# Kernel tuning notes

Measured on AMD Instinct MI355X. Metric: run time of the kernel, lower is better.

## Reference

```python
import jax, jax.numpy as jnp
import numpy as np

K = 7            # involution kernel size
GC = 16          # group_channels (hardcoded in module)
EPS = 1e-5       # BatchNorm eps


def setup_inputs() -> dict:
    key = jax.random.key(0)
    ks = jax.random.split(key, 5)
    C, R = 256, 4
    mid = C // R                      # 64
    groups = C // GC                  # 16
    B, H, W = 4, 56, 56
    x = jax.random.normal(ks[0], (B, C, H, W), dtype=jnp.float32)
    w1 = jax.random.normal(ks[1], (mid, C), dtype=jnp.float32) * (1.0 / np.sqrt(C))
    b1 = jax.random.normal(ks[2], (mid,), dtype=jnp.float32) * 0.01
    gamma = jnp.ones((mid,), dtype=jnp.float32)
    beta = jnp.zeros((mid,), dtype=jnp.float32)
    w2 = jax.random.normal(ks[3], (K * K * groups, mid), dtype=jnp.float32) * (1.0 / np.sqrt(mid))
    b2 = jax.random.normal(ks[4], (K * K * groups,), dtype=jnp.float32) * 0.01
    return {"x": x, "w1": w1, "b1": b1, "gamma": gamma, "beta": beta, "w2": w2, "b2": b2}


def reference(x, w1, b1, gamma, beta, w2, b2):
    B, C, H, W = x.shape
    groups = C // GC
    k2 = K * K
    pad = (K - 1) // 2

    # weight branch: 1x1 conv -> BN (batch stats, training-mode math) -> ReLU -> 1x1 conv
    t = jnp.einsum('oc,bchw->bohw', w1, x) + b1[None, :, None, None]
    mu = t.mean(axis=(0, 2, 3), keepdims=True)
    var = ((t - mu) ** 2).mean(axis=(0, 2, 3), keepdims=True)
    t = (t - mu) * jax.lax.rsqrt(var + EPS)
    t = t * gamma[None, :, None, None] + beta[None, :, None, None]
    t = jax.nn.relu(t)
    wgt = jnp.einsum('ot,bthw->bohw', w2, t) + b2[None, :, None, None]
    wgt = wgt.reshape(B, groups, k2, H, W)              # per-pixel kernels

    # unfold: kernel positions row-major (i over kh, j over kw), channel-major layout
    xp = jnp.pad(x, ((0, 0), (0, 0), (pad, pad), (pad, pad)))
    patches = jnp.stack(
        [xp[:, :, i:i + H, j:j + W] for i in range(K) for j in range(K)], axis=2
    )                                                   # [B, C, k2, H, W]
    patches = patches.reshape(B, groups, GC, k2, H, W)

    out = jnp.einsum('bgkhw,bgckhw->bgchw', wgt, patches)  # weighted sum over k2
    return out.reshape(B, C, H, W)
```

## Files before the change

kernel.cpp:

```cpp
#include <hip/hip_runtime.h>

#define KSZ   7
#define KK    49
#define GCH   16
#define CIN   256
#define MID   64
#define NGRP  16
#define WID   56
#define HWSZ  3136
#define NB    4
#define NPIX  (NB * HWSZ)
#define EPSV  1e-5f


__global__ __launch_bounds__(256) void k1_conv1(const float* __restrict__ x,
                                                const float* __restrict__ w1,
                                                const float* __restrict__ b1,
                                                float* __restrict__ ws) {
    const int tid = threadIdx.x;
    const int pix = blockIdx.x * 256 + tid;
    const int ob  = blockIdx.y * 4;
    const int b   = pix / HWSZ;
    const int hw  = pix - b * HWSZ;

    float acc[4];
#pragma unroll
    for (int i = 0; i < 4; ++i) acc[i] = b1[ob + i];

    const float* xp = x + (size_t)b * CIN * HWSZ + hw;
#pragma unroll 16
    for (int c = 0; c < CIN; ++c) {
        const float xv = xp[(size_t)c * HWSZ];
#pragma unroll
        for (int i = 0; i < 4; ++i)
            acc[i] = fmaf(w1[(ob + i) * CIN + c], xv, acc[i]);
    }

    float* tp = ws + 256 + (size_t)ob * NPIX + pix;
#pragma unroll
    for (int i = 0; i < 4; ++i) tp[(size_t)i * NPIX] = acc[i];

    __shared__ float bs[4];
    __shared__ float bq[4];
    if (tid < 4) { bs[tid] = 0.f; bq[tid] = 0.f; }
    __syncthreads();

#pragma unroll
    for (int i = 0; i < 4; ++i) {
        float s = acc[i];
        float q = acc[i] * acc[i];
#pragma unroll
        for (int m = 1; m < 64; m <<= 1) {
            s += __shfl_xor(s, m, 64);
            q += __shfl_xor(q, m, 64);
        }
        if ((tid & 63) == 0) {
            atomicAdd(&bs[i], s);
            atomicAdd(&bq[i], q);
        }
    }
    __syncthreads();
    if (tid < 4) {
        atomicAdd(&ws[ob + tid],      bs[tid]);
        atomicAdd(&ws[64 + ob + tid], bq[tid]);
    }
}

__global__ void k2_stats(float* __restrict__ ws,
                         const float* __restrict__ gamma,
                         const float* __restrict__ beta) {
    const int o = threadIdx.x;
    const float n   = (float)NPIX;
    const float mu  = ws[o] / n;
    const float var = ws[64 + o] / n - mu * mu;
    const float a   = gamma[o] * rsqrtf(var + EPSV);
    ws[128 + o] = a;
    ws[192 + o] = beta[o] - mu * a;
}

__global__ __launch_bounds__(256) void k3_fused(const float* __restrict__ x,
                                                const float* __restrict__ w2,
                                                const float* __restrict__ b2,
                                                const float* __restrict__ ws,
                                                float* __restrict__ out) {
    __shared__ float tl[MID][128];
    const int tid  = threadIdx.x;
    const int p    = tid & 127;
    const int half = __builtin_amdgcn_readfirstlane(tid >> 7);
    const int pix  = blockIdx.x * 128 + p;
    const int g    = blockIdx.y * 2 + half;
    const int b    = pix / HWSZ;
    const int hw   = pix - b * HWSZ;
    const int h    = hw / WID;
    const int w    = hw - h * WID;

    {
        const float* tcol = ws + 256 + blockIdx.x * 128 + p;
#pragma unroll 8
        for (int i = 0; i < 32; ++i) {
            const int o = half * 32 + i;
            const float v = tcol[(size_t)o * NPIX];
            tl[o][p] = fmaxf(0.f, fmaf(ws[128 + o], v, ws[192 + o]));
        }
    }
    __syncthreads();

    float acc[GCH];
#pragma unroll
    for (int cc = 0; cc < GCH; ++cc) acc[cc] = 0.f;

    const float* w2g = w2 + (size_t)g * KK * MID;
    const float* b2g = b2 + (size_t)g * KK;
    const int   xbase = (b * CIN + g * GCH) * HWSZ;

    for (int kc = 0; kc < 7; ++kc) {
        float aw[7];
#pragma unroll
        for (int j = 0; j < 7; ++j) aw[j] = b2g[kc * 7 + j];

#pragma unroll 8
        for (int o = 0; o < MID; ++o) {
            const float tv = tl[o][p];
#pragma unroll
            for (int j = 0; j < 7; ++j)
                aw[j] = fmaf(w2g[(kc * 7 + j) * MID + o], tv, aw[j]);
        }

        const int  hh    = h + kc - 3;
        const bool rowok = (unsigned)hh < 56u;
#pragma unroll
        for (int j = 0; j < 7; ++j) {
            const int  ww = w + j - 3;
            const bool ok = rowok && ((unsigned)ww < 56u);
            const float wm = ok ? aw[j] : 0.f;
            const int  off = ok ? (hh * WID + ww) : 0;
            const float* xb = x + xbase + off;
#pragma unroll
            for (int cc = 0; cc < GCH; ++cc)
                acc[cc] = fmaf(wm, xb[(size_t)cc * HWSZ], acc[cc]);
        }
    }

    float* ob = out + (size_t)xbase + hw;
#pragma unroll
    for (int cc = 0; cc < GCH; ++cc) ob[(size_t)cc * HWSZ] = acc[cc];
}

extern "C" void kernel_launch(void* const* d_in, const int* in_sizes, int n_in,
                              void* d_out, int out_size, void* d_ws, size_t ws_size,
                              hipStream_t stream) {
    const float* x     = (const float*)d_in[0];
    const float* w1    = (const float*)d_in[1];
    const float* b1    = (const float*)d_in[2];
    const float* gamma = (const float*)d_in[3];
    const float* beta  = (const float*)d_in[4];
    const float* w2    = (const float*)d_in[5];
    const float* b2    = (const float*)d_in[6];
    float* out = (float*)d_out;
    float* ws  = (float*)d_ws;

    hipMemsetAsync(ws, 0, 128 * sizeof(float), stream);

    k1_conv1<<<dim3(49, 16), 256, 0, stream>>>(x, w1, b1, ws);
    k2_stats<<<1, 64, 0, stream>>>(ws, gamma, beta);
    k3_fused<<<dim3(98, 8), 256, 0, stream>>>(x, w2, b2, ws, out);
}
```

Before: 104.0 us.

## Split involution kernel generation and aggregation across four waves via shared memory

Each block now handles one group with 512 threads. The four 128-thread quarters first compute disjoint slices of the 49 per-pixel kernel weights into shared memory. After a barrier, each quarter aggregates 4 of the group's 16 channels using those shared weights. This spreads the per-thread work of the second 1x1 conv and raises parallelism, at the cost of more shared memory (about 57KB per block), an extra barrier, and reloading the relu'd t tile per group.

```diff
diff --git a/kernel.cpp b/kernel.cpp
--- a/kernel.cpp
+++ b/kernel.cpp
@@ -78,72 +78,88 @@
     ws[192 + o] = beta[o] - mu * a;
 }
 
-__global__ __launch_bounds__(256) void k3_fused(const float* __restrict__ x,
+template <int T0, int NT>
+__device__ inline void phaseA(const float* __restrict__ w2g,
+                              const float* __restrict__ b2g,
+                              const float (*__restrict__ tl)[128],
+                              float (*__restrict__ wgt)[128], int p) {
+    float aw[NT];
+#pragma unroll
+    for (int t = 0; t < NT; ++t) aw[t] = b2g[T0 + t];
+#pragma unroll
+    for (int oc = 0; oc < MID; oc += 8) {
+        float tv[8];
+#pragma unroll
+        for (int i = 0; i < 8; ++i) tv[i] = tl[oc + i][p];
+#pragma unroll
+        for (int t = 0; t < NT; ++t)
+#pragma unroll
+            for (int i = 0; i < 8; ++i)
+                aw[t] = fmaf(w2g[(T0 + t) * MID + oc + i], tv[i], aw[t]);
+    }
+#pragma unroll
+    for (int t = 0; t < NT; ++t) wgt[T0 + t][p] = aw[t];
+}
+
+__global__ __launch_bounds__(512) void k3_fused(const float* __restrict__ x,
                                                 const float* __restrict__ w2,
                                                 const float* __restrict__ b2,
                                                 const float* __restrict__ ws,
                                                 float* __restrict__ out) {
     __shared__ float tl[MID][128];
-    const int tid  = threadIdx.x;
-    const int p    = tid & 127;
-    const int half = __builtin_amdgcn_readfirstlane(tid >> 7);
-    const int pix  = blockIdx.x * 128 + p;
-    const int g    = blockIdx.y * 2 + half;
-    const int b    = pix / HWSZ;
-    const int hw   = pix - b * HWSZ;
-    const int h    = hw / WID;
-    const int w    = hw - h * WID;
+    __shared__ float wgt[KK][128];
+    const int tid = threadIdx.x;
+    const int p   = tid & 127;
+    const int q   = __builtin_amdgcn_readfirstlane(tid >> 7);
+    const int pix = blockIdx.x * 128 + p;
+    const int g   = blockIdx.y;
+    const int b   = pix / HWSZ;
+    const int hw  = pix - b * HWSZ;
+    const int h   = hw / WID;
+    const int w   = hw - h * WID;
 
     {
         const float* tcol = ws + 256 + blockIdx.x * 128 + p;
-#pragma unroll 8
-        for (int i = 0; i < 32; ++i) {
-            const int o = half * 32 + i;
+#pragma unroll
+        for (int i = 0; i < 16; ++i) {
+            const int o = q * 16 + i;
             const float v = tcol[(size_t)o * NPIX];
             tl[o][p] = fmaxf(0.f, fmaf(ws[128 + o], v, ws[192 + o]));
         }
     }
     __syncthreads();
 
-    float acc[GCH];
-#pragma unroll
-    for (int cc = 0; cc < GCH; ++cc) acc[cc] = 0.f;
-
     const float* w2g = w2 + (size_t)g * KK * MID;
     const float* b2g = b2 + (size_t)g * KK;
-    const int   xbase = (b * CIN + g * GCH) * HWSZ;
 
-    for (int kc = 0; kc < 7; ++kc) {
-        float aw[7];
+    if      (q == 0) phaseA< 0, 12>(w2g, b2g, tl, wgt, p);
+    else if (q == 1) phaseA<12, 12>(w2g, b2g, tl, wgt, p);
+    else if (q == 2) phaseA<24, 12>(w2g, b2g, tl, wgt, p);
+    else             phaseA<36, 13>(w2g, b2g, tl, wgt, p);
+    __syncthreads();
+
+    float acc[4] = {0.f, 0.f, 0.f, 0.f};
+    const int xbase = (b * CIN + g * GCH + q * 4) * HWSZ;
+
 #pragma unroll
-        for (int j = 0; j < 7; ++j) aw[j] = b2g[kc * 7 + j];
-
-#pragma unroll 8
-        for (int o = 0; o < MID; ++o) {
-            const float tv = tl[o][p];
+    for (int t = 0; t < KK; ++t) {
+        const int di = t / 7 - 3;
+        const int dj = t % 7 - 3;
+        const int hh = h + di;
+        const int ww = w + dj;
+        const bool ok = ((unsigned)hh < 56u) && ((unsigned)ww < 56u);
+        const float wv = wgt[t][p];
+        const float wm = ok ? wv : 0.f;
+        const int  off = ok ? (hh * WID + ww) : 0;
+        const float* xb = x + xbase + off;
 #pragma unroll
-            for (int j = 0; j < 7; ++j)
-                aw[j] = fmaf(w2g[(kc * 7 + j) * MID + o], tv, aw[j]);
-        }
-
-        const int  hh    = h + kc - 3;
-        const bool rowok = (unsigned)hh < 56u;
-#pragma unroll
-        for (int j = 0; j < 7; ++j) {
-            const int  ww = w + j - 3;
-            const bool ok = rowok && ((unsigned)ww < 56u);
-            const float wm = ok ? aw[j] : 0.f;
-            const int  off = ok ? (hh * WID + ww) : 0;
-            const float* xb = x + xbase + off;
-#pragma unroll
-            for (int cc = 0; cc < GCH; ++cc)
-                acc[cc] = fmaf(wm, xb[(size_t)cc * HWSZ], acc[cc]);
-        }
+        for (int cc = 0; cc < 4; ++cc)
+            acc[cc] = fmaf(wm, xb[(size_t)cc * HWSZ], acc[cc]);
     }
 
     float* ob = out + (size_t)xbase + hw;
 #pragma unroll
-    for (int cc = 0; cc < GCH; ++cc) ob[(size_t)cc * HWSZ] = acc[cc];
+    for (int cc = 0; cc < 4; ++cc) ob[(size_t)cc * HWSZ] = acc[cc];
 }
 
 extern "C" void kernel_launch(void* const* d_in, const int* in_sizes, int n_in,
@@ -163,5 +179,5 @@
 
     k1_conv1<<<dim3(49, 16), 256, 0, stream>>>(x, w1, b1, ws);
     k2_stats<<<1, 64, 0, stream>>>(ws, gamma, beta);
-    k3_fused<<<dim3(98, 8), 256, 0, stream>>>(x, w2, b2, ws, out);
+    k3_fused<<<dim3(98, 16), 512, 0, stream>>>(x, w2, b2, ws, out);
 }
```

Result: faster. 100.2 us (-3.7%).

## Compute per-pixel involution weights with bf16 MFMA and split channels across threads

Applied to the files above, without the earlier changes.

The second 1x1 conv (weight generation) in the fused kernel now uses bf16 MFMA 16x16x32 instructions on LDS-staged activations and weights, replacing the scalar FMA loops. Per-pixel kernels are staged in shared memory, and each block now handles one group with 512 threads, each thread doing 4 channels of the 7x7 weighted sum. A new transpose kernel lays w1 out so conv1 can read it with float4 loads. This trades precision (bf16 weight generation) for tensor throughput and adds an extra kernel launch.

```diff
diff --git a/kernel.cpp b/kernel.cpp
--- a/kernel.cpp
+++ b/kernel.cpp
@@ -1,4 +1,8 @@
 #include <hip/hip_runtime.h>
+#include <hip/hip_bf16.h>
+
+typedef short bf16x8 __attribute__((ext_vector_type(8)));
+typedef float f32x4  __attribute__((ext_vector_type(4)));
 
 #define KSZ   7
 #define KK    49
@@ -12,9 +16,18 @@
 #define NPIX  (NB * HWSZ)
 #define EPSV  1e-5f
 
+#define WS_W1T 256
+#define WS_T   (256 + CIN * MID)
+
+__global__ __launch_bounds__(256) void k0_transpose(const float* __restrict__ w1,
+                                                    float* __restrict__ ws) {
+    const int i = blockIdx.x * 256 + threadIdx.x;
+    const int c = i >> 6;
+    const int o = i & 63;
+    ws[WS_W1T + i] = w1[o * CIN + c];
+}
 
 __global__ __launch_bounds__(256) void k1_conv1(const float* __restrict__ x,
-                                                const float* __restrict__ w1,
                                                 const float* __restrict__ b1,
                                                 float* __restrict__ ws) {
     const int tid = threadIdx.x;
@@ -28,15 +41,18 @@
     for (int i = 0; i < 4; ++i) acc[i] = b1[ob + i];
 
     const float* xp = x + (size_t)b * CIN * HWSZ + hw;
+    const float* wT = ws + WS_W1T + ob;
 #pragma unroll 16
     for (int c = 0; c < CIN; ++c) {
-        const float xv = xp[(size_t)c * HWSZ];
-#pragma unroll
-        for (int i = 0; i < 4; ++i)
-            acc[i] = fmaf(w1[(ob + i) * CIN + c], xv, acc[i]);
-    }
-
-    float* tp = ws + 256 + (size_t)ob * NPIX + pix;
+        const float4 wv = *(const float4*)(wT + c * MID);
+        const float  xv = xp[(size_t)c * HWSZ];
+        acc[0] = fmaf(wv.x, xv, acc[0]);
+        acc[1] = fmaf(wv.y, xv, acc[1]);
+        acc[2] = fmaf(wv.z, xv, acc[2]);
+        acc[3] = fmaf(wv.w, xv, acc[3]);
+    }
+
+    float* tp = ws + WS_T + (size_t)ob * NPIX + pix;
 #pragma unroll
     for (int i = 0; i < 4; ++i) tp[(size_t)i * NPIX] = acc[i];
 
@@ -44,20 +60,16 @@
     __shared__ float bq[4];
     if (tid < 4) { bs[tid] = 0.f; bq[tid] = 0.f; }
     __syncthreads();
-
 #pragma unroll
     for (int i = 0; i < 4; ++i) {
         float s = acc[i];
-        float q = acc[i] * acc[i];
+        float qq = acc[i] * acc[i];
 #pragma unroll
         for (int m = 1; m < 64; m <<= 1) {
-            s += __shfl_xor(s, m, 64);
-            q += __shfl_xor(q, m, 64);
-        }
-        if ((tid & 63) == 0) {
-            atomicAdd(&bs[i], s);
-            atomicAdd(&bq[i], q);
-        }
+            s  += __shfl_xor(s, m, 64);
+            qq += __shfl_xor(qq, m, 64);
+        }
+        if ((tid & 63) == 0) { atomicAdd(&bs[i], s); atomicAdd(&bq[i], qq); }
     }
     __syncthreads();
     if (tid < 4) {
@@ -78,72 +90,110 @@
     ws[192 + o] = beta[o] - mu * a;
 }
 
-__global__ __launch_bounds__(256) void k3_fused(const float* __restrict__ x,
+__global__ __launch_bounds__(512) void k3_fused(const float* __restrict__ x,
                                                 const float* __restrict__ w2,
                                                 const float* __restrict__ b2,
                                                 const float* __restrict__ ws,
                                                 float* __restrict__ out) {
-    __shared__ float tl[MID][128];
+    __shared__ unsigned short tlb[128][72];
+    __shared__ unsigned short wb[64][72];
+    __shared__ float swgt[128][52];
     const int tid  = threadIdx.x;
     const int p    = tid & 127;
-    const int half = __builtin_amdgcn_readfirstlane(tid >> 7);
+    const int q    = tid >> 7;
+    const int lane = tid & 63;
+    const int wave = tid >> 6;
+    const int g    = blockIdx.y;
     const int pix  = blockIdx.x * 128 + p;
-    const int g    = blockIdx.y * 2 + half;
-    const int b    = pix / HWSZ;
-    const int hw   = pix - b * HWSZ;
-    const int h    = hw / WID;
-    const int w    = hw - h * WID;
 
     {
-        const float* tcol = ws + 256 + blockIdx.x * 128 + p;
-#pragma unroll 8
-        for (int i = 0; i < 32; ++i) {
-            const int o = half * 32 + i;
-            const float v = tcol[(size_t)o * NPIX];
-            tl[o][p] = fmaxf(0.f, fmaf(ws[128 + o], v, ws[192 + o]));
-        }
-    }
-    __syncthreads();
-
-    float acc[GCH];
-#pragma unroll
-    for (int cc = 0; cc < GCH; ++cc) acc[cc] = 0.f;
-
-    const float* w2g = w2 + (size_t)g * KK * MID;
-    const float* b2g = b2 + (size_t)g * KK;
-    const int   xbase = (b * CIN + g * GCH) * HWSZ;
-
-    for (int kc = 0; kc < 7; ++kc) {
-        float aw[7];
-#pragma unroll
-        for (int j = 0; j < 7; ++j) aw[j] = b2g[kc * 7 + j];
-
-#pragma unroll 8
-        for (int o = 0; o < MID; ++o) {
-            const float tv = tl[o][p];
-#pragma unroll
-            for (int j = 0; j < 7; ++j)
-                aw[j] = fmaf(w2g[(kc * 7 + j) * MID + o], tv, aw[j]);
-        }
-
-        const int  hh    = h + kc - 3;
-        const bool rowok = (unsigned)hh < 56u;
+        const float* tcol = ws + WS_T + blockIdx.x * 128 + p;
+        bf16x8 v0, v1;
+#pragma unroll
+        for (int i = 0; i < 16; ++i) {
+            const int o = q * 16 + i;
+            float v = tcol[(size_t)o * NPIX];
+            v = fmaxf(0.f, fmaf(ws[128 + o], v, ws[192 + o]));
+            __hip_bfloat16 hb = __float2bfloat16(v);
+            const short s = *reinterpret_cast<short*>(&hb);
+            if (i < 8) v0[i & 7] = s; else v1[i & 7] = s;
+        }
+        *(bf16x8*)&tlb[p][q * 16]     = v0;
+        *(bf16x8*)&tlb[p][q * 16 + 8] = v1;
+    }
+
+    for (int e = tid; e < 64 * 64; e += 512) {
+        const int row = e >> 6;
+        const int k   = e & 63;
+        const float v = (row < KK) ? w2[((size_t)g * KK + row) * MID + k] : 0.f;
+        __hip_bfloat16 hb = __float2bfloat16(v);
+        wb[row][k] = *reinterpret_cast<unsigned short*>(&hb);
+    }
+    __syncthreads();
+
+    {
+        const int m  = wave >> 1;
+        const int n0 = (wave & 1) * 4;
+        const int r  = lane & 15;
+        const int hi = lane >> 4;
+        f32x4 acc[4] = {{0,0,0,0},{0,0,0,0},{0,0,0,0},{0,0,0,0}};
+#pragma unroll
+        for (int ks = 0; ks < 2; ++ks) {
+            const bf16x8 af = *(const bf16x8*)&wb[m * 16 + r][ks * 32 + hi * 8];
+#pragma unroll
+            for (int ni = 0; ni < 4; ++ni) {
+                const bf16x8 bfv = *(const bf16x8*)&tlb[(n0 + ni) * 16 + r][ks * 32 + hi * 8];
+                acc[ni] = __builtin_amdgcn_mfma_f32_16x16x32_bf16(af, bfv, acc[ni], 0, 0, 0);
+            }
+        }
+#pragma unroll
+        for (int ni = 0; ni < 4; ++ni) {
+            const int px = (n0 + ni) * 16 + r;
+#pragma unroll
+            for (int j = 0; j < 4; ++j) {
+                const int tap = m * 16 + hi * 4 + j;
+                if (tap < KK) swgt[px][tap] = acc[ni][j];
+            }
+        }
+    }
+    __syncthreads();
+
+    const int b  = pix / HWSZ;
+    const int hw = pix - b * HWSZ;
+    const int h  = hw / WID;
+    const int w  = hw - h * WID;
+    const float* xq   = x + ((size_t)b * CIN + g * GCH + q * 4) * HWSZ;
+    const float* bias = b2 + g * KK;
+
+    float a0 = 0.f, a1 = 0.f, a2 = 0.f, a3 = 0.f;
+    bool colok[7];
+#pragma unroll
+    for (int j = 0; j < 7; ++j) colok[j] = (unsigned)(w + j - 3) < 56u;
+
+#pragma unroll
+    for (int r7 = 0; r7 < 7; ++r7) {
+        const bool rowok = (unsigned)(h + r7 - 3) < 56u;
+        const int  roff  = hw + (r7 - 3) * WID - 3;
 #pragma unroll
         for (int j = 0; j < 7; ++j) {
-            const int  ww = w + j - 3;
-            const bool ok = rowok && ((unsigned)ww < 56u);
-            const float wm = ok ? aw[j] : 0.f;
-            const int  off = ok ? (hh * WID + ww) : 0;
-            const float* xb = x + xbase + off;
-#pragma unroll
-            for (int cc = 0; cc < GCH; ++cc)
-                acc[cc] = fmaf(wm, xb[(size_t)cc * HWSZ], acc[cc]);
-        }
-    }
-
-    float* ob = out + (size_t)xbase + hw;
-#pragma unroll
-    for (int cc = 0; cc < GCH; ++cc) ob[(size_t)cc * HWSZ] = acc[cc];
+            const int   t   = r7 * 7 + j;
+            const float wgv = swgt[p][t] + bias[t];
+            const float wm  = (rowok && colok[j]) ? wgv : 0.f;
+            int idx = roff + j;
+            idx = idx < 0 ? 0 : idx;
+            idx = idx > (HWSZ - 1) ? (HWSZ - 1) : idx;
+            a0 = fmaf(wm, xq[idx],            a0);
+            a1 = fmaf(wm, xq[idx + HWSZ],     a1);
+            a2 = fmaf(wm, xq[idx + 2 * HWSZ], a2);
+            a3 = fmaf(wm, xq[idx + 3 * HWSZ], a3);
+        }
+    }
+
+    float* ob = out + ((size_t)b * CIN + g * GCH + q * 4) * HWSZ + hw;
+    ob[0]        = a0;
+    ob[HWSZ]     = a1;
+    ob[2 * HWSZ] = a2;
+    ob[3 * HWSZ] = a3;
 }
 
 extern "C" void kernel_launch(void* const* d_in, const int* in_sizes, int n_in,
@@ -161,7 +211,8 @@
 
     hipMemsetAsync(ws, 0, 128 * sizeof(float), stream);
 
-    k1_conv1<<<dim3(49, 16), 256, 0, stream>>>(x, w1, b1, ws);
+    k0_transpose<<<dim3(64), 256, 0, stream>>>(w1, ws);
+    k1_conv1<<<dim3(49, 16), 256, 0, stream>>>(x, b1, ws);
     k2_stats<<<1, 64, 0, stream>>>(ws, gamma, beta);
-    k3_fused<<<dim3(98, 8), 256, 0, stream>>>(x, w2, b2, ws, out);
-}
+    k3_fused<<<dim3(98, 16), 512, 0, stream>>>(x, w2, b2, ws, out);
+}
```

Result: faster. 101.0 us (-2.8%).
